# Kernel tuning notes

Hardware: AMD Instinct MI355X
Metric: run time of the kernel (lower is better)

## Reference

```python
import jax, jax.numpy as jnp
from jax import lax
import numpy as np

B, S, D, H = 256, 2048, 16, 128
HH = H // 2  # head hidden = 64


def _p(key, shape, scale=0.05):
    return scale * jax.random.normal(key, shape, dtype=jnp.float32)


def setup_inputs() -> dict:
    key = jax.random.key(0)
    ks = jax.random.split(key, 12)
    return {
        "x": jax.random.normal(ks[0], (B, S, D), dtype=jnp.float32),
        # LSTM layer 0 (PyTorch gate order: i, f, g, o along the 4H axis)
        "W_ih0": _p(ks[1], (4 * H, D)),
        "W_hh0": _p(ks[2], (4 * H, H)),
        "b_ih0": jnp.zeros((4 * H,), jnp.float32),
        "b_hh0": jnp.zeros((4 * H,), jnp.float32),
        # LSTM layer 1
        "W_ih1": _p(ks[3], (4 * H, H)),
        "W_hh1": _p(ks[4], (4 * H, H)),
        "b_ih1": jnp.zeros((4 * H,), jnp.float32),
        "b_hh1": jnp.zeros((4 * H,), jnp.float32),
        # return head: Linear(H, H//2) -> LeakyReLU -> Linear(H//2, 1)
        "Wr1": _p(ks[5], (HH, H)), "br1": jnp.zeros((HH,), jnp.float32),
        "Wr2": _p(ks[6], (1, HH)), "br2": jnp.zeros((1,), jnp.float32),
        # vol head: Linear -> LeakyReLU -> Linear -> Softplus
        "Wv1": _p(ks[7], (HH, H)), "bv1": jnp.zeros((HH,), jnp.float32),
        "Wv2": _p(ks[8], (1, HH)), "bv2": jnp.zeros((1,), jnp.float32),
    }


def _lstm_layer(x, W_ih, W_hh, b_ih, b_hh):
    # x: (B, S, Din) -> hs: (B, S, H); PyTorch gate order i, f, g, o
    b, s, _ = x.shape
    h_dim = W_hh.shape[1]
    xg = jnp.einsum('bsd,gd->bsg', x, W_ih) + (b_ih + b_hh)  # (B, S, 4H)

    def step(carry, xg_t):
        h, c = carry
        g = xg_t + h @ W_hh.T
        i, f, gc, o = jnp.split(g, 4, axis=-1)
        i = jax.nn.sigmoid(i)
        f = jax.nn.sigmoid(f)
        gc = jnp.tanh(gc)
        o = jax.nn.sigmoid(o)
        c = f * c + i * gc
        h = o * jnp.tanh(c)
        return (h, c), h

    h0 = jnp.zeros((b, h_dim), x.dtype)
    (hN, cN), hs = lax.scan(step, (h0, jnp.zeros_like(h0)), jnp.swapaxes(xg, 0, 1))
    return jnp.swapaxes(hs, 0, 1), hN, cN


def reference(x, W_ih0, W_hh0, b_ih0, b_hh0, W_ih1, W_hh1, b_ih1, b_hh1,
              Wr1, br1, Wr2, br2, Wv1, bv1, Wv2, bv2):
    h1, hN0, cN0 = _lstm_layer(x, W_ih0, W_hh0, b_ih0, b_hh0)
    # inter-layer dropout is inactive at inference (eval mode)
    h2, hN1, cN1 = _lstm_layer(h1, W_ih1, W_hh1, b_ih1, b_hh1)
    # return head
    r = jax.nn.leaky_relu(jnp.einsum('bsh,kh->bsk', h2, Wr1) + br1)
    returns = jnp.einsum('bsk,ok->bso', r, Wr2) + br2
    # volatility head
    v = jax.nn.leaky_relu(jnp.einsum('bsh,kh->bsk', h2, Wv1) + bv1)
    volatility = jax.nn.softplus(jnp.einsum('bsk,ok->bso', v, Wv2) + bv2)
    hidden_h = jnp.stack([hN0, hN1], axis=0)  # (num_layers, B, H)
    hidden_c = jnp.stack([cN0, cN1], axis=0)
    return returns, volatility, hidden_h, hidden_c
```

## Files before the change

kernel.cpp:

```cpp
#include <hip/hip_runtime.h>
#include <hip/hip_bf16.h>

#define B_ 256
#define S_ 2048
#define D_ 16
#define H_ 128

typedef unsigned int u32;
typedef _Float16 h2t __attribute__((ext_vector_type(2)));

#define RET0 ((size_t)0)
#define VOL0 ((size_t)524288)
#define HH0  ((size_t)1048576)
#define HC0  ((size_t)1114112)

__device__ __forceinline__ float fdot2(u32 a, u32 b, float c) {
    return __builtin_amdgcn_fdot2(__builtin_bit_cast(h2t, a),
                                  __builtin_bit_cast(h2t, b), c, false);
}
__device__ __forceinline__ u32 packh2(float a, float b) {
    h2t h; h[0] = (_Float16)a; h[1] = (_Float16)b;
    return __builtin_bit_cast(u32, h);
}
__device__ __forceinline__ float sigm(float x) {
    return __builtin_amdgcn_rcpf(1.f + __builtin_amdgcn_exp2f(-1.44269504f * x));
}
__device__ __forceinline__ float tanh_(float x) {
    return 2.f * __builtin_amdgcn_rcpf(1.f + __builtin_amdgcn_exp2f(-2.88539008f * x)) - 1.f;
}
__device__ __forceinline__ float softplus_(float x) {
    if (x > 20.f) return x;
    const float e = __builtin_amdgcn_exp2f(1.44269504f * x);
    return 0.69314718f * __builtin_amdgcn_logf(1.f + e);
}
__device__ __forceinline__ float dnb1(float a) {
    return __builtin_bit_cast(float, __builtin_amdgcn_update_dpp(
        0, __builtin_bit_cast(int, a), 0xB1, 0xF, 0xF, true));
}

__global__ __launch_bounds__(512, 2) void k_l0(
    const float* __restrict__ x, const float* __restrict__ Wih,
    const float* __restrict__ Whh, const float* __restrict__ bih,
    const float* __restrict__ bhh, u32* __restrict__ h1out,
    float* __restrict__ out)
{
    __shared__ u32 xp2[2][2048];
    __shared__ float gates[2][4][128][4];
    __shared__ u32 hb[8][16];
    __shared__ u32 och[2][2048];

    const int tid = threadIdx.x, b = blockIdx.x;
    const int ksl = tid >> 7, m = tid & 127;
    const int wv = tid >> 6, j = tid & 63;
    const int unit = (ksl << 5) + (j & 31);

    u32 wx[8], wh[64];
#pragma unroll
    for (int g = 0; g < 4; ++g) {
        const int row = g * H_ + m;
        const float4 fx = *(const float4*)(Wih + row * D_ + ksl * 4);
        wx[g * 2]     = packh2(fx.x, fx.y);
        wx[g * 2 + 1] = packh2(fx.z, fx.w);
        const float4* whr = (const float4*)(Whh + row * H_ + ksl * 32);
#pragma unroll
        for (int q = 0; q < 8; ++q) {
            const float4 f = whr[q];
            wh[g * 16 + 2 * q]     = packh2(f.x, f.y);
            wh[g * 16 + 2 * q + 1] = packh2(f.z, f.w);
        }
    }
    const float bias0 = bih[unit] + bhh[unit];
    const float bias1 = bih[128 + unit] + bhh[128 + unit];
    const float bias2 = bih[256 + unit] + bhh[256 + unit];
    const float bias3 = bih[384 + unit] + bhh[384 + unit];

    const float* xb = x + (size_t)b * S_ * D_;
#pragma unroll
    for (int k = 0; k < 2; ++k) {
        const int i = tid + k * 512;
        const float4 v = *(const float4*)(xb + i * 4);
        xp2[0][2 * i]     = packh2(v.x, v.y);
        xp2[0][2 * i + 1] = packh2(v.z, v.w);
    }
    if (tid < 128) ((u32*)hb)[tid] = 0u;
    float c = 0.f;
    __syncthreads();

    for (int t = 0; t < S_; ++t) {
        if ((t & 255) == 0 && t < S_ - 256) {
            const int nw = (t >> 8) + 1;
#pragma unroll
            for (int k = 0; k < 2; ++k) {
                const int i = tid + k * 512;
                const float4 v = *(const float4*)(xb + (size_t)nw * 4096 + i * 4);
                xp2[nw & 1][2 * i]     = packh2(v.x, v.y);
                xp2[nw & 1][2 * i + 1] = packh2(v.z, v.w);
            }
        }
        const uint2 xv = *(const uint2*)&xp2[(t >> 8) & 1][(t & 255) * 8 + ksl * 2];
        const uint4* hq = (const uint4*)hb[wv];
        const uint4 h0 = hq[0], h1 = hq[1], h2 = hq[2], h3 = hq[3];
        float a0 = fdot2(xv.x, wx[0], 0.f); a0 = fdot2(xv.y, wx[1], a0);
        float a1 = fdot2(xv.x, wx[2], 0.f); a1 = fdot2(xv.y, wx[3], a1);
        float a2 = fdot2(xv.x, wx[4], 0.f); a2 = fdot2(xv.y, wx[5], a2);
        float a3 = fdot2(xv.x, wx[6], 0.f); a3 = fdot2(xv.y, wx[7], a3);
#define DG(vv, p)                                                              \
        a0 = fdot2(vv, wh[p], a0);        a1 = fdot2(vv, wh[16 + (p)], a1);    \
        a2 = fdot2(vv, wh[32 + (p)], a2); a3 = fdot2(vv, wh[48 + (p)], a3);
        DG(h0.x, 0) DG(h0.y, 1) DG(h0.z, 2) DG(h0.w, 3)
        DG(h1.x, 4) DG(h1.y, 5) DG(h1.z, 6) DG(h1.w, 7)
        DG(h2.x, 8) DG(h2.y, 9) DG(h2.z, 10) DG(h2.w, 11)
        DG(h3.x, 12) DG(h3.y, 13) DG(h3.z, 14) DG(h3.w, 15)
#undef DG
        float4 part; part.x = a0; part.y = a1; part.z = a2; part.w = a3;
        *(float4*)&gates[t & 1][ksl][m][0] = part;
        __syncthreads();
        if ((t & 31) == 0 && t) {
            u32* dst = h1out + ((size_t)b * S_ + (t - 32)) * 64;
            *(uint4*)(dst + tid * 4) = *(const uint4*)&och[((t >> 5) & 1) ^ 1][tid * 4];
        }
        const float4 s0 = *(const float4*)&gates[t & 1][0][unit][0];
        const float4 s1 = *(const float4*)&gates[t & 1][1][unit][0];
        const float4 s2 = *(const float4*)&gates[t & 1][2][unit][0];
        const float4 s3 = *(const float4*)&gates[t & 1][3][unit][0];
        const float ig = sigm((s0.x + s1.x) + (s2.x + s3.x) + bias0);
        const float fg = sigm((s0.y + s1.y) + (s2.y + s3.y) + bias1);
        const float gc = tanh_((s0.z + s1.z) + (s2.z + s3.z) + bias2);
        const float og = sigm((s0.w + s1.w) + (s2.w + s3.w) + bias3);
        c = fg * c + ig * gc;
        const float h = og * tanh_(c);
        const u32 pp = packh2(h, dnb1(h));
        if ((j & 33) == 0) {
            hb[wv][j >> 1] = pp;
            if (!(wv & 1)) och[(t >> 5) & 1][(t & 31) * 64 + (unit >> 1)] = pp;
        }
        if (t == S_ - 1 && !(wv & 1) && j < 32) {
            out[HH0 + (size_t)b * H_ + unit] = h;
            out[HC0 + (size_t)b * H_ + unit] = c;
        }
    }
    __syncthreads();
    {
        u32* dst = h1out + ((size_t)b * S_ + (S_ - 32)) * 64;
        *(uint4*)(dst + tid * 4) = *(const uint4*)&och[1][tid * 4];
    }
}

__global__ __launch_bounds__(512, 2) void k_l1(
    u32* __restrict__ hws,
    const float* __restrict__ Wih, const float* __restrict__ Whh,
    const float* __restrict__ bih, const float* __restrict__ bhh,
    float* __restrict__ out)
{
    __shared__ u32 h1w[2][5120];
    __shared__ float gates[2][4][128][4];
    __shared__ u32 hb[8][32];
    __shared__ u32 och[2][2048];

    const int tid = threadIdx.x, b = blockIdx.x;
    const int ksl = tid >> 7, m = tid & 127;
    const int wv = tid >> 6, j = tid & 63;
    const int unit = ((ksl & 1) << 6) + j;

    u32 w[128];
    const float* Wsel = (ksl < 2) ? Wih : Whh;
    const int eb = (ksl & 1) * 64;
#pragma unroll
    for (int g = 0; g < 4; ++g) {
        const int row = g * H_ + m;
        const float4* wr_ = (const float4*)(Wsel + row * H_ + eb);
#pragma unroll
        for (int q = 0; q < 16; ++q) {
            const float4 f = wr_[q];
            w[g * 32 + 2 * q]     = packh2(f.x, f.y);
            w[g * 32 + 2 * q + 1] = packh2(f.z, f.w);
        }
    }
    const float bias0 = bih[unit] + bhh[unit];
    const float bias1 = bih[128 + unit] + bhh[128 + unit];
    const float bias2 = bih[256 + unit] + bhh[256 + unit];
    const float bias3 = bih[384 + unit] + bhh[384 + unit];

    u32* hbase = hws + (size_t)b * S_ * 64;
#pragma unroll
    for (int k = 0; k < 2; ++k) {
        const int i = tid + k * 512;
        const uint4 v = *(const uint4*)(hbase + i * 4);
        *(uint4*)&h1w[0][(i >> 4) * 80 + ((i & 15) >> 2) * 20 + (i & 3) * 4] = v;
    }
    if (tid < 256) ((u32*)hb)[tid] = 0u;
    float c = 0.f;
    __syncthreads();

    for (int u = 0; u < S_; ++u) {
        uint4 v0, v1, v2, v3, v4, v5, v6, v7;
        if (ksl < 2) {
            const u32* src = &h1w[(u >> 6) & 1][(u & 63) * 80 + ksl * 40];
            v0 = *(const uint4*)(src);      v1 = *(const uint4*)(src + 4);
            v2 = *(const uint4*)(src + 8);  v3 = *(const uint4*)(src + 12);
            v4 = *(const uint4*)(src + 20); v5 = *(const uint4*)(src + 24);
            v6 = *(const uint4*)(src + 28); v7 = *(const uint4*)(src + 32);
        } else {
            const u32* src = hb[wv];
            v0 = *(const uint4*)(src);      v1 = *(const uint4*)(src + 4);
            v2 = *(const uint4*)(src + 8);  v3 = *(const uint4*)(src + 12);
            v4 = *(const uint4*)(src + 16); v5 = *(const uint4*)(src + 20);
            v6 = *(const uint4*)(src + 24); v7 = *(const uint4*)(src + 28);
        }
        float a0 = 0.f, a1 = 0.f, a2 = 0.f, a3 = 0.f;
#define DQ(vv, q4)                                                             \
        a0 = fdot2(vv.x, w[q4], a0);          a0 = fdot2(vv.y, w[(q4)+1], a0); \
        a0 = fdot2(vv.z, w[(q4)+2], a0);      a0 = fdot2(vv.w, w[(q4)+3], a0); \
        a1 = fdot2(vv.x, w[32+(q4)], a1);     a1 = fdot2(vv.y, w[33+(q4)], a1);\
        a1 = fdot2(vv.z, w[34+(q4)], a1);     a1 = fdot2(vv.w, w[35+(q4)], a1);\
        a2 = fdot2(vv.x, w[64+(q4)], a2);     a2 = fdot2(vv.y, w[65+(q4)], a2);\
        a2 = fdot2(vv.z, w[66+(q4)], a2);     a2 = fdot2(vv.w, w[67+(q4)], a2);\
        a3 = fdot2(vv.x, w[96+(q4)], a3);     a3 = fdot2(vv.y, w[97+(q4)], a3);\
        a3 = fdot2(vv.z, w[98+(q4)], a3);     a3 = fdot2(vv.w, w[99+(q4)], a3);
        DQ(v0, 0) DQ(v1, 4) DQ(v2, 8) DQ(v3, 12)
        DQ(v4, 16) DQ(v5, 20) DQ(v6, 24) DQ(v7, 28)
#undef DQ
        float4 part; part.x = a0; part.y = a1; part.z = a2; part.w = a3;
        *(float4*)&gates[u & 1][ksl][m][0] = part;
        __syncthreads();
        if ((u & 31) == 0 && u && wv < 2) {
            u32* dst = hbase + (size_t)(u - 32) * 64;
            const u32* sb = och[((u >> 5) & 1) ^ 1];
            const int t0 = tid & 127;
#pragma unroll
            for (int k = 0; k < 4; ++k)
                *(uint4*)(dst + (t0 + k * 128) * 4) =
                    *(const uint4*)(sb + (t0 + k * 128) * 4);
        }
        if ((u & 63) == 32 && u + 32 < S_ && wv < 2) {
            const int nw = (u >> 6) + 1;
            const u32* sw = hbase + (size_t)nw * 4096;
            u32* dw = h1w[nw & 1];
            const int t0 = tid & 127;
#pragma unroll
            for (int k = 0; k < 8; ++k) {
                const int i = t0 + k * 128;
                *(uint4*)&dw[(i >> 4) * 80 + ((i & 15) >> 2) * 20 + (i & 3) * 4] =
                    *(const uint4*)(sw + i * 4);
            }
        }
        if (ksl >= 2) {
            const float4 s0 = *(const float4*)&gates[u & 1][0][unit][0];
            const float4 s1 = *(const float4*)&gates[u & 1][1][unit][0];
            const float4 s2 = *(const float4*)&gates[u & 1][2][unit][0];
            const float4 s3 = *(const float4*)&gates[u & 1][3][unit][0];
            const float ig = sigm((s0.x + s1.x) + (s2.x + s3.x) + bias0);
            const float fg = sigm((s0.y + s1.y) + (s2.y + s3.y) + bias1);
            const float gc = tanh_((s0.z + s1.z) + (s2.z + s3.z) + bias2);
            const float og = sigm((s0.w + s1.w) + (s2.w + s3.w) + bias3);
            c = fg * c + ig * gc;
            const float h = og * tanh_(c);
            const u32 pp = packh2(h, dnb1(h));
            if (!(j & 1)) {
                hb[wv][j >> 1] = pp;
                if (!(wv & 1)) och[(u >> 5) & 1][(u & 31) * 64 + (unit >> 1)] = pp;
            }
            if (u == S_ - 1 && !(wv & 1)) {
                out[HH0 + 32768 + (size_t)b * H_ + unit] = h;
                out[HC0 + 32768 + (size_t)b * H_ + unit] = c;
            }
        }
    }
    __syncthreads();
    {
        u32* dst = hbase + (size_t)(S_ - 32) * 64;
        *(uint4*)(dst + tid * 4) = *(const uint4*)&och[1][tid * 4];
    }
}

__global__ __launch_bounds__(256) void k_heads(
    const u32* __restrict__ h2p,
    const float* __restrict__ Wr1, const float* __restrict__ br1,
    const float* __restrict__ Wr2, const float* __restrict__ br2,
    const float* __restrict__ Wv1, const float* __restrict__ bv1,
    const float* __restrict__ Wv2, const float* __restrict__ bv2,
    float* __restrict__ out)
{
    __shared__ u32 wr[64 * 64], wv[64 * 64];
    __shared__ float w2r[64], w2v[64], b1r[64], b1v[64];

    const int tid = threadIdx.x;
    for (int i = tid; i < 4096; i += 256) {
        wr[i] = packh2(Wr1[2 * i], Wr1[2 * i + 1]);
        wv[i] = packh2(Wv1[2 * i], Wv1[2 * i + 1]);
    }
    if (tid < 64) {
        w2r[tid] = Wr2[tid]; w2v[tid] = Wv2[tid];
        b1r[tid] = br1[tid]; b1v[tid] = bv1[tid];
    }
    __syncthreads();

    const size_t bs = (size_t)blockIdx.x * 256 + tid;
    u32 hq[64];
    const u32* src = h2p + bs * 64;
#pragma unroll
    for (int j4 = 0; j4 < 16; ++j4) {
        const uint4 v = *(const uint4*)(src + j4 * 4);
        hq[j4 * 4] = v.x; hq[j4 * 4 + 1] = v.y;
        hq[j4 * 4 + 2] = v.z; hq[j4 * 4 + 3] = v.w;
    }
    float ret = br2[0], vol = bv2[0];
    for (int k = 0; k < 64; ++k) {
        float r = b1r[k], v = b1v[k];
#pragma unroll
        for (int j = 0; j < 64; ++j) r = fdot2(hq[j], wr[k * 64 + j], r);
#pragma unroll
        for (int j = 0; j < 64; ++j) v = fdot2(hq[j], wv[k * 64 + j], v);
        r = r > 0.f ? r : 0.01f * r;
        v = v > 0.f ? v : 0.01f * v;
        ret += r * w2r[k];
        vol += v * w2v[k];
    }
    out[RET0 + bs] = ret;
    out[VOL0 + bs] = softplus_(vol);
}

extern "C" void kernel_launch(void* const* d_in, const int* in_sizes, int n_in,
                              void* d_out, int out_size, void* d_ws, size_t ws_size,
                              hipStream_t stream) {
    (void)in_sizes; (void)n_in; (void)out_size; (void)ws_size;
    const float* x    = (const float*)d_in[0];
    const float* Wih0 = (const float*)d_in[1];
    const float* Whh0 = (const float*)d_in[2];
    const float* bih0 = (const float*)d_in[3];
    const float* bhh0 = (const float*)d_in[4];
    const float* Wih1 = (const float*)d_in[5];
    const float* Whh1 = (const float*)d_in[6];
    const float* bih1 = (const float*)d_in[7];
    const float* bhh1 = (const float*)d_in[8];
    const float* Wr1  = (const float*)d_in[9];
    const float* br1  = (const float*)d_in[10];
    const float* Wr2  = (const float*)d_in[11];
    const float* br2  = (const float*)d_in[12];
    const float* Wv1  = (const float*)d_in[13];
    const float* bv1  = (const float*)d_in[14];
    const float* Wv2  = (const float*)d_in[15];
    const float* bv2  = (const float*)d_in[16];
    u32* hws  = (u32*)d_ws;
    float* out = (float*)d_out;

    k_l0<<<B_, 512, 0, stream>>>(x, Wih0, Whh0, bih0, bhh0, hws, out);
    k_l1<<<B_, 512, 0, stream>>>(hws, Wih1, Whh1, bih1, bhh1, out);
    k_heads<<<2048, 256, 0, stream>>>(hws, Wr1, br1, Wr2, br2,
                                      Wv1, bv1, Wv2, bv2, out);
}
```

Before: 3.438 ms.

## Fuse output heads into layer-1 LSTM kernel with 1024-thread blocks

Merges the layer-1 recurrence and the return/volatility heads into one kernel. Each step's hidden state is consumed by otherwise idle threads that compute the head MLPs one step behind, and results are staged in shared memory and written out at the end. The block grows to 1024 threads, with the K dimension split 8 ways and only 64 weight registers per thread, and the h2 write-back to workspace plus the separate heads launch are removed. The cost is an 8-way gate reduction done by 128 threads each step, extra head work on the serial step path, and one large block per batch row on the CU.

```diff
diff --git a/kernel.cpp b/kernel.cpp
--- a/kernel.cpp
+++ b/kernel.cpp
@@ -36,6 +36,14 @@
 __device__ __forceinline__ float dnb1(float a) {
     return __builtin_bit_cast(float, __builtin_amdgcn_update_dpp(
         0, __builtin_bit_cast(int, a), 0xB1, 0xF, 0xF, true));
+}
+__device__ __forceinline__ float dxor1(float a) {
+    return __builtin_bit_cast(float, __builtin_amdgcn_update_dpp(
+        0, __builtin_bit_cast(int, a), 0xB1, 0xF, 0xF, true));
+}
+__device__ __forceinline__ float dxor2(float a) {
+    return __builtin_bit_cast(float, __builtin_amdgcn_update_dpp(
+        0, __builtin_bit_cast(int, a), 0x4E, 0xF, 0xF, true));
 }
 
 __global__ __launch_bounds__(512, 2) void k_l0(
@@ -146,178 +154,198 @@
     }
 }
 
-__global__ __launch_bounds__(512, 2) void k_l1(
-    u32* __restrict__ hws,
+__global__ __launch_bounds__(1024) void k_l1h(
+    const u32* __restrict__ hws,
     const float* __restrict__ Wih, const float* __restrict__ Whh,
     const float* __restrict__ bih, const float* __restrict__ bhh,
-    float* __restrict__ out)
-{
-    __shared__ u32 h1w[2][5120];
-    __shared__ float gates[2][4][128][4];
-    __shared__ u32 hb[8][32];
-    __shared__ u32 och[2][2048];
-
-    const int tid = threadIdx.x, b = blockIdx.x;
-    const int ksl = tid >> 7, m = tid & 127;
-    const int wv = tid >> 6, j = tid & 63;
-    const int unit = ((ksl & 1) << 6) + j;
-
-    u32 w[128];
-    const float* Wsel = (ksl < 2) ? Wih : Whh;
-    const int eb = (ksl & 1) * 64;
-#pragma unroll
-    for (int g = 0; g < 4; ++g) {
-        const int row = g * H_ + m;
-        const float4* wr_ = (const float4*)(Wsel + row * H_ + eb);
-#pragma unroll
-        for (int q = 0; q < 16; ++q) {
-            const float4 f = wr_[q];
-            w[g * 32 + 2 * q]     = packh2(f.x, f.y);
-            w[g * 32 + 2 * q + 1] = packh2(f.z, f.w);
-        }
-    }
-    const float bias0 = bih[unit] + bhh[unit];
-    const float bias1 = bih[128 + unit] + bhh[128 + unit];
-    const float bias2 = bih[256 + unit] + bhh[256 + unit];
-    const float bias3 = bih[384 + unit] + bhh[384 + unit];
-
-    u32* hbase = hws + (size_t)b * S_ * 64;
-#pragma unroll
-    for (int k = 0; k < 2; ++k) {
-        const int i = tid + k * 512;
-        const uint4 v = *(const uint4*)(hbase + i * 4);
-        *(uint4*)&h1w[0][(i >> 4) * 80 + ((i & 15) >> 2) * 20 + (i & 3) * 4] = v;
-    }
-    if (tid < 256) ((u32*)hb)[tid] = 0u;
-    float c = 0.f;
-    __syncthreads();
-
-    for (int u = 0; u < S_; ++u) {
-        uint4 v0, v1, v2, v3, v4, v5, v6, v7;
-        if (ksl < 2) {
-            const u32* src = &h1w[(u >> 6) & 1][(u & 63) * 80 + ksl * 40];
-            v0 = *(const uint4*)(src);      v1 = *(const uint4*)(src + 4);
-            v2 = *(const uint4*)(src + 8);  v3 = *(const uint4*)(src + 12);
-            v4 = *(const uint4*)(src + 20); v5 = *(const uint4*)(src + 24);
-            v6 = *(const uint4*)(src + 28); v7 = *(const uint4*)(src + 32);
-        } else {
-            const u32* src = hb[wv];
-            v0 = *(const uint4*)(src);      v1 = *(const uint4*)(src + 4);
-            v2 = *(const uint4*)(src + 8);  v3 = *(const uint4*)(src + 12);
-            v4 = *(const uint4*)(src + 16); v5 = *(const uint4*)(src + 20);
-            v6 = *(const uint4*)(src + 24); v7 = *(const uint4*)(src + 28);
-        }
-        float a0 = 0.f, a1 = 0.f, a2 = 0.f, a3 = 0.f;
-#define DQ(vv, q4)                                                             \
-        a0 = fdot2(vv.x, w[q4], a0);          a0 = fdot2(vv.y, w[(q4)+1], a0); \
-        a0 = fdot2(vv.z, w[(q4)+2], a0);      a0 = fdot2(vv.w, w[(q4)+3], a0); \
-        a1 = fdot2(vv.x, w[32+(q4)], a1);     a1 = fdot2(vv.y, w[33+(q4)], a1);\
-        a1 = fdot2(vv.z, w[34+(q4)], a1);     a1 = fdot2(vv.w, w[35+(q4)], a1);\
-        a2 = fdot2(vv.x, w[64+(q4)], a2);     a2 = fdot2(vv.y, w[65+(q4)], a2);\
-        a2 = fdot2(vv.z, w[66+(q4)], a2);     a2 = fdot2(vv.w, w[67+(q4)], a2);\
-        a3 = fdot2(vv.x, w[96+(q4)], a3);     a3 = fdot2(vv.y, w[97+(q4)], a3);\
-        a3 = fdot2(vv.z, w[98+(q4)], a3);     a3 = fdot2(vv.w, w[99+(q4)], a3);
-        DQ(v0, 0) DQ(v1, 4) DQ(v2, 8) DQ(v3, 12)
-        DQ(v4, 16) DQ(v5, 20) DQ(v6, 24) DQ(v7, 28)
-#undef DQ
-        float4 part; part.x = a0; part.y = a1; part.z = a2; part.w = a3;
-        *(float4*)&gates[u & 1][ksl][m][0] = part;
-        __syncthreads();
-        if ((u & 31) == 0 && u && wv < 2) {
-            u32* dst = hbase + (size_t)(u - 32) * 64;
-            const u32* sb = och[((u >> 5) & 1) ^ 1];
-            const int t0 = tid & 127;
-#pragma unroll
-            for (int k = 0; k < 4; ++k)
-                *(uint4*)(dst + (t0 + k * 128) * 4) =
-                    *(const uint4*)(sb + (t0 + k * 128) * 4);
-        }
-        if ((u & 63) == 32 && u + 32 < S_ && wv < 2) {
-            const int nw = (u >> 6) + 1;
-            const u32* sw = hbase + (size_t)nw * 4096;
-            u32* dw = h1w[nw & 1];
-            const int t0 = tid & 127;
-#pragma unroll
-            for (int k = 0; k < 8; ++k) {
-                const int i = t0 + k * 128;
-                *(uint4*)&dw[(i >> 4) * 80 + ((i & 15) >> 2) * 20 + (i & 3) * 4] =
-                    *(const uint4*)(sw + i * 4);
-            }
-        }
-        if (ksl >= 2) {
-            const float4 s0 = *(const float4*)&gates[u & 1][0][unit][0];
-            const float4 s1 = *(const float4*)&gates[u & 1][1][unit][0];
-            const float4 s2 = *(const float4*)&gates[u & 1][2][unit][0];
-            const float4 s3 = *(const float4*)&gates[u & 1][3][unit][0];
-            const float ig = sigm((s0.x + s1.x) + (s2.x + s3.x) + bias0);
-            const float fg = sigm((s0.y + s1.y) + (s2.y + s3.y) + bias1);
-            const float gc = tanh_((s0.z + s1.z) + (s2.z + s3.z) + bias2);
-            const float og = sigm((s0.w + s1.w) + (s2.w + s3.w) + bias3);
-            c = fg * c + ig * gc;
-            const float h = og * tanh_(c);
-            const u32 pp = packh2(h, dnb1(h));
-            if (!(j & 1)) {
-                hb[wv][j >> 1] = pp;
-                if (!(wv & 1)) och[(u >> 5) & 1][(u & 31) * 64 + (unit >> 1)] = pp;
-            }
-            if (u == S_ - 1 && !(wv & 1)) {
-                out[HH0 + 32768 + (size_t)b * H_ + unit] = h;
-                out[HC0 + 32768 + (size_t)b * H_ + unit] = c;
-            }
-        }
-    }
-    __syncthreads();
-    {
-        u32* dst = hbase + (size_t)(S_ - 32) * 64;
-        *(uint4*)(dst + tid * 4) = *(const uint4*)&och[1][tid * 4];
-    }
-}
-
-__global__ __launch_bounds__(256) void k_heads(
-    const u32* __restrict__ h2p,
     const float* __restrict__ Wr1, const float* __restrict__ br1,
     const float* __restrict__ Wr2, const float* __restrict__ br2,
     const float* __restrict__ Wv1, const float* __restrict__ bv1,
     const float* __restrict__ Wv2, const float* __restrict__ bv2,
     float* __restrict__ out)
 {
-    __shared__ u32 wr[64 * 64], wv[64 * 64];
-    __shared__ float w2r[64], w2v[64], b1r[64], b1v[64];
-
-    const int tid = threadIdx.x;
-    for (int i = tid; i < 4096; i += 256) {
-        wr[i] = packh2(Wr1[2 * i], Wr1[2 * i + 1]);
-        wv[i] = packh2(Wv1[2 * i], Wv1[2 * i + 1]);
-    }
-    if (tid < 64) {
-        w2r[tid] = Wr2[tid]; w2v[tid] = Wv2[tid];
-        b1r[tid] = br1[tid]; b1v[tid] = bv1[tid];
-    }
-    __syncthreads();
-
-    const size_t bs = (size_t)blockIdx.x * 256 + tid;
-    u32 hq[64];
-    const u32* src = h2p + bs * 64;
-#pragma unroll
-    for (int j4 = 0; j4 < 16; ++j4) {
-        const uint4 v = *(const uint4*)(src + j4 * 4);
-        hq[j4 * 4] = v.x; hq[j4 * 4 + 1] = v.y;
-        hq[j4 * 4 + 2] = v.z; hq[j4 * 4 + 3] = v.w;
-    }
-    float ret = br2[0], vol = bv2[0];
-    for (int k = 0; k < 64; ++k) {
-        float r = b1r[k], v = b1v[k];
-#pragma unroll
-        for (int j = 0; j < 64; ++j) r = fdot2(hq[j], wr[k * 64 + j], r);
-#pragma unroll
-        for (int j = 0; j < 64; ++j) v = fdot2(hq[j], wv[k * 64 + j], v);
-        r = r > 0.f ? r : 0.01f * r;
-        v = v > 0.f ? v : 0.01f * v;
-        ret += r * w2r[k];
-        vol += v * w2v[k];
-    }
-    out[RET0 + bs] = ret;
-    out[VOL0 + bs] = softplus_(vol);
+    __shared__ u32 h1w[64 * 80];
+    __shared__ float gates[8][128][4];
+    __shared__ u32 hp[2][80];
+    __shared__ u32 whd[8704];
+    __shared__ float redbuf[2][8];
+    __shared__ float rvr[S_], rvv[S_];
+
+    const int tid = threadIdx.x, b = blockIdx.x;
+    const int ksl = tid >> 7, m = tid & 127;
+
+    u32 w[64];
+    const float* Wsel = (ksl < 4) ? Wih : Whh;
+    const int colb = (ksl & 3) * 32;
+#pragma unroll
+    for (int g = 0; g < 4; ++g) {
+        const int row = g * H_ + m;
+        const float4* wr_ = (const float4*)(Wsel + row * H_ + colb);
+#pragma unroll
+        for (int q = 0; q < 8; ++q) {
+            const float4 f = wr_[q];
+            w[g * 16 + 2 * q]     = packh2(f.x, f.y);
+            w[g * 16 + 2 * q + 1] = packh2(f.z, f.w);
+        }
+    }
+    float bias[4], c = 0.f;
+    if (tid < 128) {
+#pragma unroll
+        for (int g = 0; g < 4; ++g) bias[g] = bih[g * H_ + tid] + bhh[g * H_ + tid];
+    }
+    const int ht = tid - 128;
+    const int head = (ht >> 8) & 1;
+    const int wk = (ht >> 6) & 3;
+    const int hk = wk * 16 + ((ht >> 2) & 15);
+    const int hq = ht & 3;
+    float b1k = 0.f, w2k = 0.f;
+    if (tid >= 128 && tid < 640) {
+        b1k = (head ? bv1 : br1)[hk];
+        w2k = (head ? Wv2 : Wr2)[hk];
+    }
+    float br2v = 0.f, bv2v = 0.f;
+    if (tid == 640) { br2v = br2[0]; bv2v = bv2[0]; }
+    for (int i = tid; i < 4096; i += 1024) {
+        const int kq = i >> 6, p = i & 63;
+        whd[kq * 68 + p]        = packh2(Wr1[i * 2], Wr1[i * 2 + 1]);
+        whd[4352 + kq * 68 + p] = packh2(Wv1[i * 2], Wv1[i * 2 + 1]);
+    }
+    if (tid < 160) ((u32*)hp)[tid] = 0u;
+    __syncthreads();
+
+    const u32* hbase = hws + (size_t)b * S_ * 64;
+    for (int u = 0; u < S_; ++u) {
+        if ((u & 63) == 0) {
+            const uint4 v = *(const uint4*)(hbase + (size_t)u * 64 + tid * 4);
+            const int st = tid >> 4, p4 = tid & 15;
+            *(uint4*)(&h1w[st * 80 + (p4 >> 2) * 20 + (p4 & 3) * 4]) = v;
+            __syncthreads();
+        }
+        const u32* sel = (ksl < 4) ? &h1w[(u & 63) * 80 + ksl * 20]
+                                   : &hp[(u + 1) & 1][(ksl - 4) * 20];
+        float a0 = 0.f, a1 = 0.f, a2 = 0.f, a3 = 0.f;
+#pragma unroll
+        for (int p = 0; p < 4; ++p) {
+            const uint4 v = *(const uint4*)(sel + p * 4);
+            a0 = fdot2(v.x, w[4 * p], a0);      a0 = fdot2(v.y, w[4 * p + 1], a0);
+            a0 = fdot2(v.z, w[4 * p + 2], a0);  a0 = fdot2(v.w, w[4 * p + 3], a0);
+            a1 = fdot2(v.x, w[16 + 4 * p], a1); a1 = fdot2(v.y, w[17 + 4 * p], a1);
+            a1 = fdot2(v.z, w[18 + 4 * p], a1); a1 = fdot2(v.w, w[19 + 4 * p], a1);
+            a2 = fdot2(v.x, w[32 + 4 * p], a2); a2 = fdot2(v.y, w[33 + 4 * p], a2);
+            a2 = fdot2(v.z, w[34 + 4 * p], a2); a2 = fdot2(v.w, w[35 + 4 * p], a2);
+            a3 = fdot2(v.x, w[48 + 4 * p], a3); a3 = fdot2(v.y, w[49 + 4 * p], a3);
+            a3 = fdot2(v.z, w[50 + 4 * p], a3); a3 = fdot2(v.w, w[51 + 4 * p], a3);
+        }
+        float4 part; part.x = a0; part.y = a1; part.z = a2; part.w = a3;
+        *(float4*)&gates[ksl][m][0] = part;
+        __syncthreads();
+        if (tid < 128) {
+            float4 s = *(const float4*)&gates[0][tid][0];
+#pragma unroll
+            for (int k = 1; k < 8; ++k) {
+                const float4 p = *(const float4*)&gates[k][tid][0];
+                s.x += p.x; s.y += p.y; s.z += p.z; s.w += p.w;
+            }
+            const float ig = sigm(s.x + bias[0]);
+            const float fg = sigm(s.y + bias[1]);
+            const float gc = tanh_(s.z + bias[2]);
+            const float og = sigm(s.w + bias[3]);
+            c = fg * c + ig * gc;
+            const float hv = og * tanh_(c);
+            const u32 pp = packh2(hv, dnb1(hv));
+            if (!(tid & 1)) {
+                const int p2 = tid >> 1;
+                hp[u & 1][(p2 >> 4) * 20 + (p2 & 15)] = pp;
+            }
+            if (u == S_ - 1) {
+                out[HH0 + 32768 + (size_t)b * H_ + tid] = hv;
+                out[HC0 + 32768 + (size_t)b * H_ + tid] = c;
+            }
+        } else if (tid < 640) {
+            if (u >= 1) {
+                const u32* hsrc = &hp[(u + 1) & 1][hq * 20];
+                const uint4 y0 = *(const uint4*)(hsrc);
+                const uint4 y1 = *(const uint4*)(hsrc + 4);
+                const uint4 y2 = *(const uint4*)(hsrc + 8);
+                const uint4 y3 = *(const uint4*)(hsrc + 12);
+                const u32* wp = &whd[head * 4352 + hk * 68 + hq * 16];
+                const uint4 w0 = *(const uint4*)(wp);
+                const uint4 w1 = *(const uint4*)(wp + 4);
+                const uint4 w2_ = *(const uint4*)(wp + 8);
+                const uint4 w3 = *(const uint4*)(wp + 12);
+                float d = 0.f;
+                d = fdot2(y0.x, w0.x, d); d = fdot2(y0.y, w0.y, d);
+                d = fdot2(y0.z, w0.z, d); d = fdot2(y0.w, w0.w, d);
+                d = fdot2(y1.x, w1.x, d); d = fdot2(y1.y, w1.y, d);
+                d = fdot2(y1.z, w1.z, d); d = fdot2(y1.w, w1.w, d);
+                d = fdot2(y2.x, w2_.x, d); d = fdot2(y2.y, w2_.y, d);
+                d = fdot2(y2.z, w2_.z, d); d = fdot2(y2.w, w2_.w, d);
+                d = fdot2(y3.x, w3.x, d); d = fdot2(y3.y, w3.y, d);
+                d = fdot2(y3.z, w3.z, d); d = fdot2(y3.w, w3.w, d);
+                d += dxor1(d); d += dxor2(d);
+                float val = 0.f;
+                if (hq == 0) {
+                    const float dd = d + b1k;
+                    val = (dd > 0.f ? dd : 0.01f * dd) * w2k;
+                }
+                val += __shfl_xor(val, 4);  val += __shfl_xor(val, 8);
+                val += __shfl_xor(val, 16); val += __shfl_xor(val, 32);
+                if ((tid & 63) == 0) redbuf[(u - 1) & 1][head * 4 + wk] = val;
+            }
+        } else if (tid == 640) {
+            if (u >= 2) {
+                const float* rb = redbuf[u & 1];
+                rvr[u - 2] = rb[0] + rb[1] + rb[2] + rb[3] + br2v;
+                rvv[u - 2] = softplus_(rb[4] + rb[5] + rb[6] + rb[7] + bv2v);
+            }
+        }
+        __syncthreads();
+    }
+    if (tid >= 128 && tid < 640) {
+        const u32* hsrc = &hp[1][hq * 20];
+        const uint4 y0 = *(const uint4*)(hsrc);
+        const uint4 y1 = *(const uint4*)(hsrc + 4);
+        const uint4 y2 = *(const uint4*)(hsrc + 8);
+        const uint4 y3 = *(const uint4*)(hsrc + 12);
+        const u32* wp = &whd[head * 4352 + hk * 68 + hq * 16];
+        const uint4 w0 = *(const uint4*)(wp);
+        const uint4 w1 = *(const uint4*)(wp + 4);
+        const uint4 w2_ = *(const uint4*)(wp + 8);
+        const uint4 w3 = *(const uint4*)(wp + 12);
+        float d = 0.f;
+        d = fdot2(y0.x, w0.x, d); d = fdot2(y0.y, w0.y, d);
+        d = fdot2(y0.z, w0.z, d); d = fdot2(y0.w, w0.w, d);
+        d = fdot2(y1.x, w1.x, d); d = fdot2(y1.y, w1.y, d);
+        d = fdot2(y1.z, w1.z, d); d = fdot2(y1.w, w1.w, d);
+        d = fdot2(y2.x, w2_.x, d); d = fdot2(y2.y, w2_.y, d);
+        d = fdot2(y2.z, w2_.z, d); d = fdot2(y2.w, w2_.w, d);
+        d = fdot2(y3.x, w3.x, d); d = fdot2(y3.y, w3.y, d);
+        d = fdot2(y3.z, w3.z, d); d = fdot2(y3.w, w3.w, d);
+        d += dxor1(d); d += dxor2(d);
+        float val = 0.f;
+        if (hq == 0) {
+            const float dd = d + b1k;
+            val = (dd > 0.f ? dd : 0.01f * dd) * w2k;
+        }
+        val += __shfl_xor(val, 4);  val += __shfl_xor(val, 8);
+        val += __shfl_xor(val, 16); val += __shfl_xor(val, 32);
+        if ((tid & 63) == 0) redbuf[1][head * 4 + wk] = val;
+    } else if (tid == 640) {
+        const float* rb = redbuf[0];
+        rvr[S_ - 2] = rb[0] + rb[1] + rb[2] + rb[3] + br2v;
+        rvv[S_ - 2] = softplus_(rb[4] + rb[5] + rb[6] + rb[7] + bv2v);
+    }
+    __syncthreads();
+    if (tid == 640) {
+        const float* rb = redbuf[1];
+        rvr[S_ - 1] = rb[0] + rb[1] + rb[2] + rb[3] + br2v;
+        rvv[S_ - 1] = softplus_(rb[4] + rb[5] + rb[6] + rb[7] + bv2v);
+    }
+    __syncthreads();
+    for (int s = tid; s < S_; s += 1024) {
+        out[RET0 + (size_t)b * S_ + s] = rvr[s];
+        out[VOL0 + (size_t)b * S_ + s] = rvv[s];
+    }
 }
 
 extern "C" void kernel_launch(void* const* d_in, const int* in_sizes, int n_in,
@@ -345,7 +373,6 @@
     float* out = (float*)d_out;
 
     k_l0<<<B_, 512, 0, stream>>>(x, Wih0, Whh0, bih0, bhh0, hws, out);
-    k_l1<<<B_, 512, 0, stream>>>(hws, Wih1, Whh1, bih1, bhh1, out);
-    k_heads<<<2048, 256, 0, stream>>>(hws, Wr1, br1, Wr2, br2,
-                                      Wv1, bv1, Wv2, bv2, out);
-}
+    k_l1h<<<B_, 1024, 0, stream>>>(hws, Wih1, Whh1, bih1, bhh1,
+                                   Wr1, br1, Wr2, br2, Wv1, bv1, Wv2, bv2, out);
+}
```

New measurement: 3.610 ms. 1.05x slower.
